# Kernel tuning notes

Hardware: AMD Instinct MI355X
Metric: run time of the kernel (lower is better)

## Reference

```python
import math
import jax
import jax.numpy as jnp
import numpy as np
from jax import lax

TOP_K = 8
SINKHORN_ITERS = 15
RADIUS = 3  # neighbor_radius of LocalGeometricValidator


def _avg_pool_nopad(x, k, pad):
    """avg_pool2d(kernel=k, stride=1, padding=pad, count_include_pad=False) on NCHW."""
    dims = (1, 1, k, k)
    strides = (1, 1, 1, 1)
    padding = ((0, 0), (0, 0), (pad, pad), (pad, pad))
    s = lax.reduce_window(x, jnp.array(0.0, x.dtype), lax.add, dims, strides, padding)
    ones = jnp.ones((1, 1) + x.shape[2:], x.dtype)
    cnt = lax.reduce_window(ones, jnp.array(0.0, x.dtype), lax.add, dims, strides, padding)
    return s / cnt


def _geo_scores(src_pos, cand_pos, H, W, radius=RADIUS):
    """src_pos [B,N,2], cand_pos [B,N,K,2] -> [B,N,K] local geometric consistency."""
    B, N, K, _ = cand_pos.shape
    src2d = src_pos.reshape(B, H, W, 2).transpose(0, 3, 1, 2)              # [B,2,H,W]
    cand = cand_pos.transpose(0, 2, 1, 3).reshape(B * K, H, W, 2)
    cand = cand.transpose(0, 3, 1, 2)                                      # [B*K,2,H,W]
    src_exp = jnp.broadcast_to(src2d[:, None], (B, K, 2, H, W)).reshape(B * K, 2, H, W)
    disp = cand - src_exp
    k = 2 * radius + 1
    mean_d = _avg_pool_nopad(disp, k, radius)
    mean_sq = _avg_pool_nopad(disp ** 2, k, radius)
    var = jnp.clip(mean_sq - mean_d ** 2, 0.0)
    total_var = var.sum(axis=1).reshape(B, K, N)                           # [B,K,N]
    score = 1.0 / (1.0 + total_var * 100.0)
    return score.transpose(0, 2, 1)                                        # [B,N,K]


def _optimal_transport(scores, temp, dustbin, iters):
    """scores [B,M,N] (already divided by temp) -> log assignment [B,M,N]."""
    s = jnp.nan_to_num(scores.astype(jnp.float32), nan=0.0, posinf=50.0, neginf=-50.0)
    s = jnp.clip(s, -50.0, 50.0)
    B, M, N = s.shape
    ds = jnp.clip(dustbin.astype(jnp.float32) / temp, -50.0, 50.0)
    row_dust = jnp.broadcast_to(ds, (B, M, 1))
    col_dust = jnp.broadcast_to(ds, (B, 1, N))
    corner = jnp.zeros((B, 1, 1), jnp.float32)
    top = jnp.concatenate([s, row_dust], axis=2)
    bot = jnp.concatenate([col_dust, corner], axis=2)
    Z = jnp.concatenate([top, bot], axis=1)                                # [B,M+1,N+1]
    norm = -math.log(M + N)
    log_mu = jnp.full((B, M + 1), norm, jnp.float32).at[:, M].set(math.log(N) + norm)
    log_nu = jnp.full((B, N + 1), norm, jnp.float32).at[:, N].set(math.log(M) + norm)

    Zd = lax.stop_gradient(Z)  # torch.no_grad() loop

    def body(carry, _):
        u, v = carry
        u = log_mu - jax.nn.logsumexp(Zd + v[:, None, :], axis=2)
        v = log_nu - jax.nn.logsumexp(Zd + u[:, :, None], axis=1)
        return (u, v), None

    (u, v), _ = lax.scan(body, (jnp.zeros_like(log_mu), jnp.zeros_like(log_nu)),
                         None, length=iters - 1)
    # final differentiable iteration
    u = log_mu - jax.nn.logsumexp(Z + v[:, None, :], axis=2)
    v = log_nu - jax.nn.logsumexp(Z + u[:, :, None], axis=1)
    log_assign = Z + u[:, :, None] + v[:, None, :]
    log_assign = jnp.nan_to_num(log_assign, nan=-50.0, posinf=0.0, neginf=-50.0)
    return log_assign[:, :M, :N]


def _l2norm(x, eps=1e-12):
    n = jnp.sqrt(jnp.sum(x * x, axis=-1, keepdims=True))
    return x / jnp.maximum(n, eps)


def _forward(feat_A, feat_B, pos_A, pos_B, dustbin_score, geo_weight, current_temp, H, W):
    B, N, C = feat_A.shape
    norm_A = _l2norm(feat_A)
    norm_B = _l2norm(feat_B)
    raw_sim = jnp.einsum('bmc,bnc->bmn', norm_A, norm_B)                   # [B,N,N]
    scores = raw_sim / current_temp
    temp = jnp.clip(current_temp.astype(jnp.float32), 0.03, 10.0)
    log_assign = _optimal_transport(scores, temp, dustbin_score, SINKHORN_ITERS)
    M, Ncols = log_assign.shape[1], log_assign.shape[2]

    ot_prob = jnp.exp(jnp.clip(log_assign.astype(jnp.float32), -50.0, 0.0))
    ot_prob = jnp.nan_to_num(ot_prob, nan=0.0, posinf=1.0, neginf=0.0)
    row_mass = jnp.maximum(ot_prob.sum(axis=-1, keepdims=True), 1e-8)
    prob_dist = ot_prob / row_mass
    valid_prob_sum = jnp.clip(row_mass * float(M + Ncols), 0.0, 1.0)

    base_expected = jnp.einsum('bmn,bnd->bmd', prob_dist, pos_B)           # [B,N,2]

    _, topk_idx = lax.top_k(ot_prob, TOP_K)                                # [B,N,K]
    bidx = jnp.arange(B)[:, None, None]
    topk_positions = pos_B[bidx, topk_idx]                                 # [B,N,K,2]

    geo_scores = _geo_scores(pos_A, topk_positions, H, W)                  # [B,N,K]
    gw = jnp.clip(geo_weight, 0.0, 2.0)

    topk_logp, _ = lax.top_k(log_assign.astype(jnp.float32), TOP_K)
    combined = topk_logp + gw.astype(jnp.float32) * geo_scores.astype(jnp.float32)
    soft_w = jax.nn.softmax(combined, axis=-1)

    geo_offset = (topk_positions * soft_w[..., None]).sum(axis=2) - lax.stop_gradient(base_expected)
    refined = base_expected + geo_offset
    refined = jnp.clip(jnp.nan_to_num(refined, nan=0.0, posinf=1.5, neginf=-1.5), -1.5, 1.5)

    entropy = -(prob_dist * jnp.log(jnp.maximum(prob_dist, 1e-8))).sum(axis=-1)
    entropy = entropy * valid_prob_sum[..., 0]
    return refined, entropy, raw_sim, geo_scores


def setup_inputs() -> dict:
    key = jax.random.key(0)
    k1, k2, k3, k4 = jax.random.split(key, 4)
    B, H, W, C = 4, 64, 64, 128
    N = H * W
    feat_A = jax.random.normal(k1, (B, N, C), jnp.float32)
    feat_B = jax.random.normal(k2, (B, N, C), jnp.float32)
    pos_A = jax.random.uniform(k3, (B, N, 2), jnp.float32) * 2.0 - 1.0
    pos_B = jax.random.uniform(k4, (B, N, 2), jnp.float32) * 2.0 - 1.0
    return {
        'feat_A': feat_A, 'feat_B': feat_B, 'pos_A': pos_A, 'pos_B': pos_B,
        'dustbin_score': jnp.asarray(-1.0, jnp.float32),
        'geo_weight': jnp.asarray(0.5, jnp.float32),
        'current_temp': jnp.asarray(0.1, jnp.float32),
        'H': H, 'W': W,
    }


def reference(feat_A, feat_B, pos_A, pos_B, dustbin_score, geo_weight, current_temp, H, W):
    return _forward(feat_A, feat_B, pos_A, pos_B, dustbin_score, geo_weight, current_temp, H, W)
```

## Files before the change

### kernel.cpp

```cpp
#include <hip/hip_runtime.h>
#include <hip/hip_fp16.h>
#include <math.h>

#define NB 4
#define NN 4096
#define NC 128
#define MU (1.0f/8192.0f)
#define NBLK 128
#define NFIN 32

__global__ void scalars_k(const float* __restrict__ ds, const float* __restrict__ gw,
                          const float* __restrict__ ct, float* __restrict__ scal) {
    if (threadIdx.x == 0) {
        float t = ct[0];
        scal[0] = 1.0f / t;
        float tc = fminf(fmaxf(t, 0.03f), 10.0f);
        float d = fminf(fmaxf(ds[0] / tc, -50.0f), 50.0f);
        scal[1] = __expf(d);
        scal[2] = fminf(fmaxf(gw[0], 0.0f), 2.0f);
    }
}

__global__ __launch_bounds__(256) void invnorm_k(const float* __restrict__ fA, const float* __restrict__ fB,
                                                 float* __restrict__ invA, float* __restrict__ invB) {
    int wv = blockIdx.x * 4 + (threadIdx.x >> 6);
    int lane = threadIdx.x & 63;
    const float* src;
    float* dst;
    if (wv < NB * NN) { src = fA + (size_t)wv * NC; dst = invA + wv; }
    else              { src = fB + (size_t)(wv - NB * NN) * NC; dst = invB + (wv - NB * NN); }
    float2 x = *(const float2*)(src + 2 * lane);
    float ss = x.x * x.x + x.y * x.y;
#pragma unroll
    for (int off = 32; off; off >>= 1) ss += __shfl_down(ss, off);
    if (lane == 0) *dst = 1.0f / fmaxf(sqrtf(ss), 1e-12f);
}

__global__ __launch_bounds__(256) void gemm_k(const float* __restrict__ A, const float* __restrict__ B,
                                              const float* __restrict__ invA, const float* __restrict__ invB,
                                              float* __restrict__ sim_out) {
    __shared__ float As[16][128];
    __shared__ float Bs[16][128];
    int b = blockIdx.z;
    int m0 = blockIdx.y * 128, n0 = blockIdx.x * 128;
    const float* Ab = A + (size_t)b * NN * NC;
    const float* Bb = B + (size_t)b * NN * NC;
    int t = threadIdx.x;
    int tr = t >> 2, tq = t & 3;
    int ty = t >> 4, tx = t & 15;
    float acc[8][8] = {};
    for (int k0 = 0; k0 < NC; k0 += 16) {
        float4 a0 = *(const float4*)(Ab + (size_t)(m0 + tr) * NC + k0 + 4 * tq);
        float4 a1 = *(const float4*)(Ab + (size_t)(m0 + tr + 64) * NC + k0 + 4 * tq);
        float4 b0 = *(const float4*)(Bb + (size_t)(n0 + tr) * NC + k0 + 4 * tq);
        float4 b1 = *(const float4*)(Bb + (size_t)(n0 + tr + 64) * NC + k0 + 4 * tq);
        __syncthreads();
        As[4 * tq + 0][tr] = a0.x; As[4 * tq + 1][tr] = a0.y; As[4 * tq + 2][tr] = a0.z; As[4 * tq + 3][tr] = a0.w;
        As[4 * tq + 0][tr + 64] = a1.x; As[4 * tq + 1][tr + 64] = a1.y; As[4 * tq + 2][tr + 64] = a1.z; As[4 * tq + 3][tr + 64] = a1.w;
        Bs[4 * tq + 0][tr] = b0.x; Bs[4 * tq + 1][tr] = b0.y; Bs[4 * tq + 2][tr] = b0.z; Bs[4 * tq + 3][tr] = b0.w;
        Bs[4 * tq + 0][tr + 64] = b1.x; Bs[4 * tq + 1][tr + 64] = b1.y; Bs[4 * tq + 2][tr + 64] = b1.z; Bs[4 * tq + 3][tr + 64] = b1.w;
        __syncthreads();
#pragma unroll
        for (int k = 0; k < 16; k++) {
            float av[8], bv[8];
            *(float4*)av = *(const float4*)&As[k][ty * 8];
            *(float4*)(av + 4) = *(const float4*)&As[k][ty * 8 + 4];
            *(float4*)bv = *(const float4*)&Bs[k][tx * 8];
            *(float4*)(bv + 4) = *(const float4*)&Bs[k][tx * 8 + 4];
#pragma unroll
            for (int i = 0; i < 8; i++)
#pragma unroll
                for (int j = 0; j < 8; j++) acc[i][j] = fmaf(av[i], bv[j], acc[i][j]);
        }
    }
    int m_base = m0 + ty * 8;
    int n_base = n0 + tx * 8;
    float ib[8];
#pragma unroll
    for (int j = 0; j < 8; j++) ib[j] = invB[(size_t)b * NN + n_base + j];
#pragma unroll
    for (int i = 0; i < 8; i++) {
        int m = m_base + i;
        float ia = invA[(size_t)b * NN + m];
        float row[8];
#pragma unroll
        for (int j = 0; j < 8; j++) row[j] = acc[i][j] * ia * ib[j];
        size_t rbase = ((size_t)b * NN + m) * NN + n_base;
        float4* so = (float4*)(sim_out + rbase);
        so[0] = make_float4(row[0], row[1], row[2], row[3]);
        so[1] = make_float4(row[4], row[5], row[6], row[7]);
    }
}

__device__ __forceinline__ float kval(float s, float ict) {
    float z = fminf(fmaxf(s * ict, -50.0f), 50.0f);
    return __expf(z);
}

__global__ void init_sink2_k(float* __restrict__ cperm, float* __restrict__ st) {
    int i = blockIdx.x * 256 + threadIdx.x;
    if (i < NB * NN) cperm[i] = 1.0f;
    if (i < NB) st[i] = 1.0f;
    if (i < NB * NFIN) st[NB + i] = (float)NN / (float)NFIN;
}

__global__ __launch_bounds__(256) void sink_rc_k(const float* __restrict__ sim,
        const float* __restrict__ cperm, const float* __restrict__ stPrev,
        float* __restrict__ r, float* __restrict__ rsum_part, float* __restrict__ colpart,
        const float* __restrict__ scal) {
    __shared__ float4 cls[1024];
    __shared__ float4 red[1024];
    __shared__ float wsum[4];
    int b = blockIdx.y, blk = blockIdx.x;
    int t = threadIdx.x, w = t >> 6, lane = t & 63;
    float kd = scal[1], ict = scal[0];
    float c_dust = stPrev[b];
    const float4* cp = (const float4*)cperm + (size_t)b * 1024;
#pragma unroll
    for (int q = 0; q < 4; q++) cls[t + 256 * q] = cp[t + 256 * q];
    __syncthreads();
    float colacc[64];
#pragma unroll
    for (int q = 0; q < 64; q++) colacc[q] = 0.0f;
    float rsum = 0.0f;
    const float* Sb = sim + (size_t)b * NN * NN;
#pragma unroll 1
    for (int i = 0; i < 8; i++) {
        int m = blk * 32 + w * 8 + i;
        const float4* Srow = (const float4*)(Sb + (size_t)m * NN);
        float kv[64];
        float acc0 = 0.0f, acc1 = 0.0f;
#pragma unroll
        for (int s = 0; s < 8; s++) {
            float4 v0 = Srow[128 * s + 2 * lane];
            float4 v1 = Srow[128 * s + 2 * lane + 1];
            float4 c0 = cls[128 * s + lane];
            float4 c1 = cls[128 * s + 64 + lane];
            float k0 = kval(v0.x, ict), k1 = kval(v0.y, ict), k2 = kval(v0.z, ict), k3 = kval(v0.w, ict);
            float k4 = kval(v1.x, ict), k5 = kval(v1.y, ict), k6 = kval(v1.z, ict), k7 = kval(v1.w, ict);
            kv[8 * s + 0] = k0; kv[8 * s + 1] = k1; kv[8 * s + 2] = k2; kv[8 * s + 3] = k3;
            kv[8 * s + 4] = k4; kv[8 * s + 5] = k5; kv[8 * s + 6] = k6; kv[8 * s + 7] = k7;
            acc0 = fmaf(k0, c0.x, acc0); acc0 = fmaf(k1, c0.y, acc0);
            acc0 = fmaf(k2, c0.z, acc0); acc0 = fmaf(k3, c0.w, acc0);
            acc1 = fmaf(k4, c1.x, acc1); acc1 = fmaf(k5, c1.y, acc1);
            acc1 = fmaf(k6, c1.z, acc1); acc1 = fmaf(k7, c1.w, acc1);
        }
        float acc = acc0 + acc1;
#pragma unroll
        for (int off = 1; off < 64; off <<= 1) acc += __shfl_xor(acc, off);
        float rm = MU / (acc + kd * c_dust);
        if (lane == 0) r[(size_t)b * NN + m] = rm;
        rsum += rm;
#pragma unroll
        for (int q = 0; q < 64; q++) colacc[q] = fmaf(kv[q], rm, colacc[q]);
    }
    if (lane == 0) wsum[w] = rsum;
    __syncthreads();
    if (w == 0) {
#pragma unroll
        for (int s = 0; s < 8; s++) {
            red[128 * s + lane]      = make_float4(colacc[8 * s + 0], colacc[8 * s + 1], colacc[8 * s + 2], colacc[8 * s + 3]);
            red[128 * s + 64 + lane] = make_float4(colacc[8 * s + 4], colacc[8 * s + 5], colacc[8 * s + 6], colacc[8 * s + 7]);
        }
    }
    __syncthreads();
    if (w == 1) {
#pragma unroll
        for (int s = 0; s < 8; s++) {
            float4 x = red[128 * s + lane];
            x.x += colacc[8 * s + 0]; x.y += colacc[8 * s + 1]; x.z += colacc[8 * s + 2]; x.w += colacc[8 * s + 3];
            red[128 * s + lane] = x;
            float4 y = red[128 * s + 64 + lane];
            y.x += colacc[8 * s + 4]; y.y += colacc[8 * s + 5]; y.z += colacc[8 * s + 6]; y.w += colacc[8 * s + 7];
            red[128 * s + 64 + lane] = y;
        }
    }
    __syncthreads();
    if (w == 2) {
#pragma unroll
        for (int s = 0; s < 8; s++) {
            float4 x = red[128 * s + lane];
            x.x += colacc[8 * s + 0]; x.y += colacc[8 * s + 1]; x.z += colacc[8 * s + 2]; x.w += colacc[8 * s + 3];
            red[128 * s + lane] = x;
            float4 y = red[128 * s + 64 + lane];
            y.x += colacc[8 * s + 4]; y.y += colacc[8 * s + 5]; y.z += colacc[8 * s + 6]; y.w += colacc[8 * s + 7];
            red[128 * s + 64 + lane] = y;
        }
    }
    __syncthreads();
    if (w == 3) {
#pragma unroll
        for (int s = 0; s < 8; s++) {
            float4 x = red[128 * s + lane];
            x.x += colacc[8 * s + 0]; x.y += colacc[8 * s + 1]; x.z += colacc[8 * s + 2]; x.w += colacc[8 * s + 3];
            red[128 * s + lane] = x;
            float4 y = red[128 * s + 64 + lane];
            y.x += colacc[8 * s + 4]; y.y += colacc[8 * s + 5]; y.z += colacc[8 * s + 6]; y.w += colacc[8 * s + 7];
            red[128 * s + 64 + lane] = y;
        }
    }
    __syncthreads();
    float4* op = (float4*)colpart + ((size_t)b * NBLK + blk) * 1024;
#pragma unroll
    for (int q = 0; q < 4; q++) op[t + 256 * q] = red[t + 256 * q];
    if (t == 0) rsum_part[b * NBLK + blk] = ((wsum[0] + wsum[1]) + wsum[2]) + wsum[3];
}

__global__ __launch_bounds__(256) void sink_cfin_k(const float* __restrict__ colpart,
        const float* __restrict__ rsum_part, const float* __restrict__ stPrev,
        float* __restrict__ cperm, float* __restrict__ stNew, const float* __restrict__ scal) {
    __shared__ float4 red[8][32];
    int b = blockIdx.y;
    int t = threadIdx.x;
    int sl = blockIdx.x * 32 + (t & 31);
    int p = t >> 5;
    float kd = scal[1];
    float c_dust_prev = stPrev[b];
    float sum_c_prev = 0.0f;
#pragma unroll
    for (int x = 0; x < NFIN; x++) sum_c_prev += stPrev[NB + b * NFIN + x];
    float r_dust = 0.5f / (kd * sum_c_prev + c_dust_prev);
    const float4* cp = (const float4*)colpart + (size_t)b * NBLK * 1024;
    float4 a = make_float4(0.0f, 0.0f, 0.0f, 0.0f);
#pragma unroll 4
    for (int k = 0; k < NBLK / 8; k++) {
        float4 x = cp[(size_t)(p * (NBLK / 8) + k) * 1024 + sl];
        a.x += x.x; a.y += x.y; a.z += x.z; a.w += x.w;
    }
    red[p][t & 31] = a;
    __syncthreads();
    if (p == 0) {
        float4 a0 = red[0][t];
#pragma unroll
        for (int q = 1; q < 8; q++) {
            float4 x = red[q][t];
            a0.x += x.x; a0.y += x.y; a0.z += x.z; a0.w += x.w;
        }
        float db = kd * r_dust;
        float4 c4 = make_float4(MU / (a0.x + db), MU / (a0.y + db), MU / (a0.z + db), MU / (a0.w + db));
        ((float4*)cperm)[(size_t)b * 1024 + sl] = c4;
        float ls = ((c4.x + c4.y) + c4.z) + c4.w;
#pragma unroll
        for (int off = 1; off < 32; off <<= 1) ls += __shfl_xor(ls, off);
        if (t == 0) {
            stNew[NB + b * NFIN + blockIdx.x] = ls;
            if (blockIdx.x == 0) {
                float sum_r = 0.0f;
#pragma unroll
                for (int blk = 0; blk < NBLK; blk++) sum_r += rsum_part[b * NBLK + blk];
                stNew[b] = 0.5f / (kd * sum_r + r_dust);
            }
        }
    }
}

__global__ void vlog_k(const float* __restrict__ cperm, float* __restrict__ vswz) {
    int i = blockIdx.x * 256 + threadIdx.x;
    int b = i >> 12, e = i & 4095;
    int j = e & 3, pslot = e >> 2;
    int s = pslot >> 7, h = (pslot >> 6) & 1, l = pslot & 63;
    int n = 512 * s + 8 * l + 4 * h + j;
    vswz[((size_t)b << 12) + ((n & 63) << 6) + (n >> 6)] = logf(cperm[i]);
}

__global__ __launch_bounds__(256) void posterior_k(const float* __restrict__ sim, const float* __restrict__ r,
                                                   const float* __restrict__ vswz, const float* __restrict__ scal,
                                                   float* __restrict__ ent_out, int* __restrict__ tk_idx,
                                                   float* __restrict__ tk_logp) {
    __shared__ float vs[NN];
    int b = blockIdx.y;
    int t = threadIdx.x;
#pragma unroll
    for (int q = 0; q < 16; q++) vs[t + 256 * q] = vswz[(size_t)b * NN + t + 256 * q];
    __syncthreads();
    float ict = scal[0];
    int warp = t >> 6, lane = t & 63;
    int wv = blockIdx.x * 4 + warp;
    const float* Sb = sim + (size_t)b * NN * NN;
    for (int j4 = 0; j4 < 4; j4++) {
        int m = wv + 1024 * j4;
        const float4* Srow = (const float4*)(Sb + (size_t)m * NN);
        float u = logf(r[(size_t)b * NN + m]);
        float mass = 0.0f, pl = 0.0f;
        float tv[8]; int ti[8];
#pragma unroll
        for (int k = 0; k < 8; k++) { tv[k] = -3.4e38f; ti[k] = 0x7fffffff; }
#pragma unroll 4
        for (int s4 = 0; s4 < 16; s4++) {
            float4 q4 = Srow[16 * lane + s4];
            float zz[4] = {q4.x, q4.y, q4.z, q4.w};
#pragma unroll
            for (int jj = 0; jj < 4; jj++) {
                int n = 64 * lane + 4 * s4 + jj;
                float s = zz[jj] * ict;
                s = fminf(fmaxf(s, -50.0f), 50.0f);
                float tt = s + vs[((4 * s4 + jj) << 6) + lane];
                float l_ = tt + u;
                float lc = fminf(fmaxf(l_, -50.0f), 0.0f);
                float pp = __expf(lc);
                mass += pp;
                pl = fmaf(pp, lc, pl);
                if (tt > tv[7]) {
                    tv[7] = tt; ti[7] = n;
#pragma unroll
                    for (int k = 7; k > 0; k--) {
                        if (tv[k] > tv[k - 1]) {
                            float tmv = tv[k]; tv[k] = tv[k - 1]; tv[k - 1] = tmv;
                            int tmi = ti[k]; ti[k] = ti[k - 1]; ti[k - 1] = tmi;
                        }
                    }
                }
            }
        }
#pragma unroll
        for (int off = 32; off; off >>= 1) {
            mass += __shfl_down(mass, off);
            pl += __shfl_down(pl, off);
        }
        float outv[8]; int outi[8];
#pragma unroll
        for (int k = 0; k < 8; k++) {
            float bv = tv[0]; int bi = ti[0];
#pragma unroll
            for (int off = 32; off; off >>= 1) {
                float ov = __shfl_down(bv, off); int oi = __shfl_down(bi, off);
                if (ov > bv || (ov == bv && oi < bi)) { bv = ov; bi = oi; }
            }
            bv = __shfl(bv, 0); bi = __shfl(bi, 0);
            outv[k] = bv; outi[k] = bi;
            if (ti[0] == bi) {
#pragma unroll
                for (int k2 = 0; k2 < 7; k2++) { tv[k2] = tv[k2 + 1]; ti[k2] = ti[k2 + 1]; }
                tv[7] = -3.4e38f; ti[7] = 0x7fffffff;
            }
        }
        if (lane == 0) {
            float rm = fmaxf(mass, 1e-8f);
            float ent = (logf(rm) * mass - pl) / rm;
            float valid = fminf(fmaxf(rm * 8192.0f, 0.0f), 1.0f);
            ent_out[(size_t)b * NN + m] = ent * valid;
            size_t base = ((size_t)b * NN + m) * 8;
#pragma unroll
            for (int k = 0; k < 8; k++) { tk_idx[base + k] = outi[k]; tk_logp[base + k] = outv[k] + u; }
        }
    }
}

__global__ __launch_bounds__(256) void geo_k(const int* __restrict__ tk_idx, const float* __restrict__ posA,
                                             const float* __restrict__ posB, float* __restrict__ geo_out) {
    __shared__ float dx[NN], dy[NN];
    int k = blockIdx.x, b = blockIdx.y;
    int t = threadIdx.x;
    const float2* pA = (const float2*)posA + (size_t)b * NN;
    const float2* pB = (const float2*)posB + (size_t)b * NN;
    for (int q = 0; q < 16; q++) {
        int n = t + 256 * q;
        int idx = tk_idx[((size_t)(b * NN + n)) * 8 + k];
        float2 pb = pB[idx];
        float2 pa = pA[n];
        dx[n] = pb.x - pa.x;
        dy[n] = pb.y - pa.y;
    }
    __syncthreads();
    for (int q = 0; q < 16; q++) {
        int n = t + 256 * q;
        int y = n >> 6, x = n & 63;
        int y0 = max(y - 3, 0), y1 = min(y + 3, 63);
        int x0 = max(x - 3, 0), x1 = min(x + 3, 63);
        float sx = 0, sxx = 0, sy = 0, syy = 0;
        for (int yy = y0; yy <= y1; yy++)
            for (int xx = x0; xx <= x1; xx++) {
                float a = dx[(yy << 6) + xx], c2 = dy[(yy << 6) + xx];
                sx += a; sxx = fmaf(a, a, sxx);
                sy += c2; syy = fmaf(c2, c2, syy);
            }
        float inv = 1.0f / (float)((y1 - y0 + 1) * (x1 - x0 + 1));
        float mx = sx * inv, my = sy * inv;
        float vx = fmaxf(sxx * inv - mx * mx, 0.0f);
        float vy = fmaxf(syy * inv - my * my, 0.0f);
        geo_out[((size_t)(b * NN + n)) * 8 + k] = 1.0f / (1.0f + (vx + vy) * 100.0f);
    }
}

__global__ __launch_bounds__(256) void refine_k(const float* __restrict__ tk_logp, const int* __restrict__ tk_idx,
                                                const float* __restrict__ geo, const float* __restrict__ posB,
                                                const float* __restrict__ scal, float* __restrict__ refined) {
    int i = blockIdx.x * 256 + threadIdx.x;
    int b = i >> 12;
    float gw = scal[2];
    const float* lp = tk_logp + (size_t)i * 8;
    const float* gs = geo + (size_t)i * 8;
    const int* ix = tk_idx + (size_t)i * 8;
    const float2* pB = (const float2*)posB + (size_t)b * NN;
    float cb[8]; float mx = -3.4e38f;
#pragma unroll
    for (int k = 0; k < 8; k++) { cb[k] = fmaf(gw, gs[k], lp[k]); mx = fmaxf(mx, cb[k]); }
    float sum = 0.0f, px = 0.0f, py = 0.0f;
#pragma unroll
    for (int k = 0; k < 8; k++) {
        float w = __expf(cb[k] - mx);
        float2 p = pB[ix[k]];
        sum += w; px = fmaf(w, p.x, px); py = fmaf(w, p.y, py);
    }
    float inv = 1.0f / sum;
    px = fminf(fmaxf(px * inv, -1.5f), 1.5f);
    py = fminf(fmaxf(py * inv, -1.5f), 1.5f);
    ((float2*)refined)[i] = make_float2(px, py);
}

extern "C" void kernel_launch(void* const* d_in, const int* in_sizes, int n_in,
                              void* d_out, int out_size, void* d_ws, size_t ws_size,
                              hipStream_t stream) {
    (void)in_sizes; (void)n_in; (void)out_size; (void)ws_size;
    const float* feat_A = (const float*)d_in[0];
    const float* feat_B = (const float*)d_in[1];
    const float* pos_A = (const float*)d_in[2];
    const float* pos_B = (const float*)d_in[3];
    const float* dsc = (const float*)d_in[4];
    const float* gwp = (const float*)d_in[5];
    const float* ctp = (const float*)d_in[6];

    float* out = (float*)d_out;
    float* out_refined = out;
    float* out_entropy = out + 32768;
    float* out_sim = out + 49152;
    float* out_geo = out + 49152 + (size_t)NB * NN * NN;

    char* ws = (char*)d_ws;
    size_t off = 0;
    float* scal = (float*)(ws + off); off += 256;
    float* invA = (float*)(ws + off); off += (size_t)NB * NN * 4;
    float* invB = (float*)(ws + off); off += (size_t)NB * NN * 4;
    float* rr   = (float*)(ws + off); off += (size_t)NB * NN * 4;
    float* cperm = (float*)(ws + off); off += (size_t)NB * NN * 4;
    float* vv   = (float*)(ws + off); off += (size_t)NB * NN * 4;
    float* stA  = (float*)(ws + off); off += 1024;
    float* stB  = (float*)(ws + off); off += 1024;
    float* rsum_part = (float*)(ws + off); off += (size_t)NB * NBLK * 4;
    int* tki = (int*)(ws + off); off += (size_t)NB * NN * 8 * 4;
    float* tkl = (float*)(ws + off); off += (size_t)NB * NN * 8 * 4;
    float* colpart = (float*)(ws + off); off += (size_t)NB * NBLK * NN * 4;

    scalars_k<<<1, 64, 0, stream>>>(dsc, gwp, ctp, scal);
    invnorm_k<<<8192, 256, 0, stream>>>(feat_A, feat_B, invA, invB);
    gemm_k<<<dim3(32, 32, NB), 256, 0, stream>>>(feat_A, feat_B, invA, invB, out_sim);
    init_sink2_k<<<64, 256, 0, stream>>>(cperm, stA);
    float* stIn = stA; float* stOut = stB;
    for (int it = 0; it < 15; it++) {
        sink_rc_k<<<dim3(NBLK, NB), 256, 0, stream>>>(out_sim, cperm, stIn, rr, rsum_part, colpart, scal);
        sink_cfin_k<<<dim3(NFIN, NB), 256, 0, stream>>>(colpart, rsum_part, stIn, cperm, stOut, scal);
        float* tmp = stIn; stIn = stOut; stOut = tmp;
    }
    vlog_k<<<64, 256, 0, stream>>>(cperm, vv);
    posterior_k<<<dim3(256, NB), 256, 0, stream>>>(out_sim, rr, vv, scal, out_entropy, tki, tkl);
    geo_k<<<dim3(8, NB), 256, 0, stream>>>(tki, pos_A, pos_B, out_geo);
    refine_k<<<64, 256, 0, stream>>>(tkl, tki, out_geo, pos_B, scal, out_refined);
}
```

Measured before the change: 1.546 ms.

## Double Sinkhorn row blocks and coalesce posterior row reads with contiguous log-v

The Sinkhorn row kernel now uses 256 blocks of 16 rows each instead of 128 blocks of 32, to raise parallelism and occupancy. The final row-sum reduction becomes a wave-wide shuffle reduction instead of a serial 128-element loop on one thread. The posterior kernel now reads each sim row with a lane-interleaved float4 pattern so accesses are coalesced, and takes log-v from a plain contiguous layout with float4 shared-memory loads instead of a swizzled one. The risk is that the top-k insertion order now follows a different n sequence, which could change tie-breaking, and twice as many partial sums must be combined.

```diff
diff --git a/kernel.cpp b/kernel.cpp
--- a/kernel.cpp
+++ b/kernel.cpp
@@ -6,7 +6,7 @@
 #define NN 4096
 #define NC 128
 #define MU (1.0f/8192.0f)
-#define NBLK 128
+#define NBLK 256
 #define NFIN 32
 
 __global__ void scalars_k(const float* __restrict__ ds, const float* __restrict__ gw,
@@ -125,8 +125,8 @@
     float rsum = 0.0f;
     const float* Sb = sim + (size_t)b * NN * NN;
 #pragma unroll 1
-    for (int i = 0; i < 8; i++) {
-        int m = blk * 32 + w * 8 + i;
+    for (int i = 0; i < 4; i++) {
+        int m = blk * 16 + w * 4 + i;
         const float4* Srow = (const float4*)(Sb + (size_t)m * NN);
         float kv[64];
         float acc0 = 0.0f, acc1 = 0.0f;
@@ -242,41 +242,43 @@
         float ls = ((c4.x + c4.y) + c4.z) + c4.w;
 #pragma unroll
         for (int off = 1; off < 32; off <<= 1) ls += __shfl_xor(ls, off);
-        if (t == 0) {
-            stNew[NB + b * NFIN + blockIdx.x] = ls;
-            if (blockIdx.x == 0) {
-                float sum_r = 0.0f;
-#pragma unroll
-                for (int blk = 0; blk < NBLK; blk++) sum_r += rsum_part[b * NBLK + blk];
-                stNew[b] = 0.5f / (kd * sum_r + r_dust);
-            }
-        }
-    }
-}
-
-__global__ void vlog_k(const float* __restrict__ cperm, float* __restrict__ vswz) {
+        if (t == 0) stNew[NB + b * NFIN + blockIdx.x] = ls;
+    }
+    if (blockIdx.x == 0 && t >= 64 && t < 128) {
+        int lane = t - 64;
+        float s4 = 0.0f;
+#pragma unroll
+        for (int q = 0; q < NBLK / 64; q++) s4 += rsum_part[b * NBLK + lane + 64 * q];
+#pragma unroll
+        for (int off = 1; off < 64; off <<= 1) s4 += __shfl_xor(s4, off);
+        if (lane == 0) stNew[b] = 0.5f / (kd * s4 + r_dust);
+    }
+}
+
+__global__ void vlog_k(const float* __restrict__ cperm, float* __restrict__ v) {
     int i = blockIdx.x * 256 + threadIdx.x;
     int b = i >> 12, e = i & 4095;
     int j = e & 3, pslot = e >> 2;
     int s = pslot >> 7, h = (pslot >> 6) & 1, l = pslot & 63;
     int n = 512 * s + 8 * l + 4 * h + j;
-    vswz[((size_t)b << 12) + ((n & 63) << 6) + (n >> 6)] = logf(cperm[i]);
+    v[((size_t)b << 12) + n] = logf(cperm[i]);
 }
 
 __global__ __launch_bounds__(256) void posterior_k(const float* __restrict__ sim, const float* __restrict__ r,
-                                                   const float* __restrict__ vswz, const float* __restrict__ scal,
+                                                   const float* __restrict__ v, const float* __restrict__ scal,
                                                    float* __restrict__ ent_out, int* __restrict__ tk_idx,
                                                    float* __restrict__ tk_logp) {
-    __shared__ float vs[NN];
+    __shared__ __align__(16) float vs[NN];
     int b = blockIdx.y;
     int t = threadIdx.x;
 #pragma unroll
-    for (int q = 0; q < 16; q++) vs[t + 256 * q] = vswz[(size_t)b * NN + t + 256 * q];
+    for (int q = 0; q < 16; q++) vs[t + 256 * q] = v[(size_t)b * NN + t + 256 * q];
     __syncthreads();
     float ict = scal[0];
     int warp = t >> 6, lane = t & 63;
     int wv = blockIdx.x * 4 + warp;
     const float* Sb = sim + (size_t)b * NN * NN;
+    const float4* vs4 = (const float4*)vs;
     for (int j4 = 0; j4 < 4; j4++) {
         int m = wv + 1024 * j4;
         const float4* Srow = (const float4*)(Sb + (size_t)m * NN);
@@ -287,14 +289,16 @@
         for (int k = 0; k < 8; k++) { tv[k] = -3.4e38f; ti[k] = 0x7fffffff; }
 #pragma unroll 4
         for (int s4 = 0; s4 < 16; s4++) {
-            float4 q4 = Srow[16 * lane + s4];
+            float4 q4 = Srow[lane + 64 * s4];
+            float4 v4 = vs4[lane + 64 * s4];
             float zz[4] = {q4.x, q4.y, q4.z, q4.w};
+            float vvv[4] = {v4.x, v4.y, v4.z, v4.w};
 #pragma unroll
             for (int jj = 0; jj < 4; jj++) {
-                int n = 64 * lane + 4 * s4 + jj;
+                int n = 4 * lane + 256 * s4 + jj;
                 float s = zz[jj] * ict;
                 s = fminf(fmaxf(s, -50.0f), 50.0f);
-                float tt = s + vs[((4 * s4 + jj) << 6) + lane];
+                float tt = s + vvv[jj];
                 float l_ = tt + u;
                 float lc = fminf(fmaxf(l_, -50.0f), 0.0f);
                 float pp = __expf(lc);
```

Measured after the change: 1.485 ms. 3.9% less time.
